# Kernel tuning notes

Measured on AMD Instinct MI355X. Metric: run time of the kernel, lower is better.

Reference implementation:

```python
import jax, jax.numpy as jnp
import numpy as np

D = 1024

def setup_inputs() -> dict:
    key = jax.random.key(0)
    ks = jax.random.split(key, 9)
    s = 1.0 / np.sqrt(D)
    x = jax.random.normal(ks[0], (4096, 8, D), dtype=jnp.float32)
    Wq = jax.random.uniform(ks[1], (D, D), jnp.float32, -s, s)
    bq = jax.random.uniform(ks[2], (D,), jnp.float32, -s, s)
    Wk = jax.random.uniform(ks[3], (D, D), jnp.float32, -s, s)
    bk = jax.random.uniform(ks[4], (D,), jnp.float32, -s, s)
    Wv = jax.random.uniform(ks[5], (D, D), jnp.float32, -s, s)
    bv = jax.random.uniform(ks[6], (D,), jnp.float32, -s, s)
    Wo = jax.random.uniform(ks[7], (D, D), jnp.float32, -s, s)
    bo = jax.random.uniform(ks[8], (D,), jnp.float32, -s, s)
    return {"x": x, "Wq": Wq, "bq": bq, "Wk": Wk, "bk": bk,
            "Wv": Wv, "bv": bv, "Wo": Wo, "bo": bo}

def reference(x, Wq, bq, Wk, bk, Wv, bv, Wo, bo):
    # x: (S, B, D) seq-first, matching torch module
    Q = jax.nn.elu(x @ Wq.T + bq) + 1.0  # (S,B,D)
    K = jax.nn.elu(x @ Wk.T + bk) + 1.0  # (S,B,D)
    V = x @ Wv.T + bv                    # (S,B,D)
    # KV = K^T V per batch: (B, D, D)
    KV = jnp.einsum('sbd,sbe->bde', K, V)
    # out = Q @ KV per batch, back to (S,B,D)
    out = jnp.einsum('sbd,bde->sbe', Q, KV)
    return out @ Wo.T + bo
```

## Files before the change

### kernel.cpp

```cpp
#include <hip/hip_runtime.h>


typedef __bf16 bf16;
typedef __attribute__((ext_vector_type(8))) __bf16 bf16x8;
typedef __attribute__((ext_vector_type(4))) __bf16 bf16x4;
typedef __attribute__((ext_vector_type(4))) float f32x4;

static constexpr int S = 4096;
static constexpr int B = 8;
static constexpr int D = 1024;
static constexpr int SB = S * B;
static constexpr long long NELEM = (long long)SB * D;

__device__ __forceinline__ void load_lds16(const bf16* g, void* l)
{
    __builtin_amdgcn_global_load_lds(
        (const __attribute__((address_space(1))) void*)g,
        (__attribute__((address_space(3))) void*)l, 16, 0, 0);
}

__global__ void cvt_f32_to_bf16(const float* __restrict__ in, bf16* __restrict__ out, int n)
{
    int i = (blockIdx.x * blockDim.x + threadIdx.x) * 4;
    int stride = gridDim.x * blockDim.x * 4;
    for (; i < n; i += stride) {
        float4 v = *(const float4*)(in + i);
        bf16x4 o;
        o[0] = (bf16)v.x; o[1] = (bf16)v.y; o[2] = (bf16)v.z; o[3] = (bf16)v.w;
        *(bf16x4*)(out + i) = o;
    }
}

__global__ __launch_bounds__(256) void cvt_transpose_1024(
    const float* __restrict__ in, bf16* __restrict__ out)
{
    __shared__ bf16 tile[64][72];
    const int e0 = blockIdx.y * 64;
    const int d0 = blockIdx.x * 64;
    const int t  = threadIdx.x;
    const int rl = t >> 3;
    const int c8 = (t & 7) * 8;
    #pragma unroll
    for (int p = 0; p < 2; ++p) {
        int r = rl + p * 32;
        float4 v0 = *(const float4*)(in + (long long)(e0 + r) * D + d0 + c8);
        float4 v1 = *(const float4*)(in + (long long)(e0 + r) * D + d0 + c8 + 4);
        tile[c8+0][r] = (bf16)v0.x; tile[c8+1][r] = (bf16)v0.y;
        tile[c8+2][r] = (bf16)v0.z; tile[c8+3][r] = (bf16)v0.w;
        tile[c8+4][r] = (bf16)v1.x; tile[c8+5][r] = (bf16)v1.y;
        tile[c8+6][r] = (bf16)v1.z; tile[c8+7][r] = (bf16)v1.w;
    }
    __syncthreads();
    #pragma unroll
    for (int p = 0; p < 2; ++p) {
        int dr = rl + p * 32;
        *(bf16x8*)(out + (long long)(d0 + dr) * D + e0 + c8) = *(bf16x8*)(&tile[dr][c8]);
    }
}

__global__ __launch_bounds__(256) void bvo_kernel(
    const float* __restrict__ Wo, const float* __restrict__ bv, float* __restrict__ bvo)
{
    const int row = blockIdx.x;
    const int t = threadIdx.x;
    float4 w = *(const float4*)(Wo + (long long)row * D + t * 4);
    float4 b = *(const float4*)(bv + t * 4);
    float s = w.x*b.x + w.y*b.y + w.z*b.z + w.w*b.w;
    __shared__ float red[256];
    red[t] = s; __syncthreads();
    for (int off = 128; off > 0; off >>= 1) {
        if (t < off) red[t] += red[t + off];
        __syncthreads();
    }
    if (t == 0) bvo[row] = red[0];
}

template<int BM, int BN, int WM, int WN, int EPI, int OUTF32, int BIASROW>
__global__ __launch_bounds__(WM * WN * 64, 2) void gemm_bt(
    const bf16* __restrict__ A, const bf16* __restrict__ Bm,
    const float* __restrict__ bias, void* __restrict__ Cout,
    int lda, int ldb, int ldc, int K,
    long long aBatch, long long bBatch, long long cBatch)
{
    constexpr int THREADS = WM * WN * 64;
    constexpr int WROWS = BM / WM, WCOLS = BN / WN;
    constexpr int MI = WROWS / 16, NI = WCOLS / 16;
    constexpr int ABYTES = BM * 64;
    constexpr int BBYTES = BN * 64;
    constexpr int BUF = ABYTES + BBYTES;

    __shared__ unsigned char smem[4 * BUF];

    const int tid  = threadIdx.x;
    const int lane = tid & 63;
    const int wave = tid >> 6;
    const int wr   = wave / WN;
    const int wc   = wave % WN;
    const int bz   = blockIdx.z;

    const int nx  = gridDim.x;
    const int bid = blockIdx.y * nx + blockIdx.x;
    const int cpx = (nx * gridDim.y) >> 3;
    const int swz = (bid & 7) * cpx + (bid >> 3);
    const long long m0 = (long long)(swz / nx) * BM;
    const long long n0 = (long long)(swz % nx) * BN;

    const bf16* Ab = A  + bz * aBatch + m0 * lda;
    const bf16* Bb = Bm + bz * bBatch + n0 * ldb;

    f32x4 acc[MI][NI] = {};
    const int NT = K >> 5;

    auto stage = [&](int t) {
        unsigned char* dst = smem + (t & 3) * BUF;
        const long long kk = (long long)t << 5;
        #pragma unroll
        for (int j = 0; j < 2; ++j) {
            const int g  = wave * 64 + lane + j * THREADS;
            const int gs = g ^ ((g >> 3) & 3);
            const int row = gs >> 2, col = (gs & 3) * 8;
            load_lds16(Ab + (long long)row * lda + kk + col,
                       dst + (wave * 64 + j * THREADS) * 16);
        }
        #pragma unroll
        for (int j = 0; j < 2; ++j) {
            const int g  = wave * 64 + lane + j * THREADS;
            const int gs = g ^ ((g >> 3) & 3);
            const int row = gs >> 2, col = (gs & 3) * 8;
            load_lds16(Bb + (long long)row * ldb + kk + col,
                       dst + ABYTES + (wave * 64 + j * THREADS) * 16);
        }
    };

    stage(0); stage(1); stage(2);

    const int ko2 = (lane >> 4) * 16;
    const int la15 = lane & 15;

    for (int t = 0; t < NT; ++t) {
        if (t + 2 < NT)      asm volatile("s_waitcnt vmcnt(8)" ::: "memory");
        else if (t + 1 < NT) asm volatile("s_waitcnt vmcnt(4)" ::: "memory");
        else                 asm volatile("s_waitcnt vmcnt(0)" ::: "memory");
        __builtin_amdgcn_s_barrier();
        asm volatile("" ::: "memory");

        if (t + 3 < NT) stage(t + 3);

        const unsigned char* buf = smem + (t & 3) * BUF;
        bf16x8 a[MI], b[NI];
        #pragma unroll
        for (int mi = 0; mi < MI; ++mi) {
            int ad = (wr * WROWS + mi * 16 + la15) * 64 + ko2;
            ad ^= ((ad >> 7) & 3) << 4;
            a[mi] = *(const bf16x8*)(buf + ad);
        }
        #pragma unroll
        for (int ni = 0; ni < NI; ++ni) {
            int ad = (wc * WCOLS + ni * 16 + la15) * 64 + ko2;
            ad ^= ((ad >> 7) & 3) << 4;
            b[ni] = *(const bf16x8*)(buf + ABYTES + ad);
        }

        __builtin_amdgcn_s_setprio(1);
        #pragma unroll
        for (int mi = 0; mi < MI; ++mi)
            #pragma unroll
            for (int ni = 0; ni < NI; ++ni)
                acc[mi][ni] = __builtin_amdgcn_mfma_f32_16x16x32_bf16(
                    a[mi], b[ni], acc[mi][ni], 0, 0, 0);
        __builtin_amdgcn_s_setprio(0);
    }

    const int crow = (lane >> 4) * 4;
    const int ccol = lane & 15;
    #pragma unroll
    for (int ni = 0; ni < NI; ++ni) {
        const long long c = n0 + wc * WCOLS + ni * 16 + ccol;
        float bcol = 0.0f;
        if (!BIASROW && bias) bcol = bias[c];
        #pragma unroll
        for (int mi = 0; mi < MI; ++mi) {
            const long long r0 = m0 + wr * WROWS + mi * 16 + crow;
            #pragma unroll
            for (int j = 0; j < 4; ++j) {
                float v = acc[mi][ni][j];
                v += BIASROW ? bias[r0 + j] : bcol;
                if (EPI == 1) v = (v > 0.0f) ? (v + 1.0f) : __expf(v);
                const long long idx = bz * cBatch + (r0 + j) * ldc + c;
                if (OUTF32) ((float*)Cout)[idx] = v;
                else        ((bf16*)Cout)[idx]  = (bf16)v;
            }
        }
    }
}

template<int EPI, int OUTF32, int BIASROW>
__global__ __launch_bounds__(512, 1) void gemm8p(
    const bf16* __restrict__ A, const bf16* __restrict__ Bm,
    const float* __restrict__ bias, void* __restrict__ Cout,
    int lda, int ldb, int ldc, int K,
    long long aBatch, long long bBatch, long long cBatch)
{
    __shared__ unsigned char smem[131072];

    const int tid  = threadIdx.x;
    const int lane = tid & 63;
    const int wave = tid >> 6;
    const int wr   = wave >> 2;
    const int wc   = wave & 3;
    const int bz   = blockIdx.z;

    const int nx  = gridDim.x;
    const int bid = blockIdx.y * nx + blockIdx.x;
    const int cpx = (nx * gridDim.y) >> 3;
    const int swzb = (bid & 7) * cpx + (bid >> 3);
    const long long m0 = (long long)(swzb / nx) * 256;
    const long long n0 = (long long)(swzb % nx) * 256;

    const bf16* Ab = A  + bz * aBatch + m0 * lda;
    const bf16* Bb = Bm + bz * bBatch + n0 * ldb;

    const int sg = (lane & 3) ^ ((lane >> 3) & 3);
    const long long srow = wave * 32 + (lane >> 2);
    const bf16* srcA = Ab + srow * lda + sg * 8;
    const bf16* srcB = Bb + srow * ldb + sg * 8;
    const int dstoff = wave * 2048;

    const int la15 = lane & 15;
    const int rsw  = (lane >> 4) ^ ((la15 >> 1) & 3);
    const int a16  = (wr * 128 + la15) * 4 + rsw;
    const int b16  = (wc * 64  + la15) * 4 + rsw;

    f32x4 acc[8][4] = {};
    const int NT = K >> 6;
    const int NI = NT >> 1;

    auto stageA = [&](int T, int kh) {
        const int reg = ((((T & 1) << 1) | kh) << 14);
        const long long kp = ((long long)T << 6) + (kh << 5);
        load_lds16(srcA + kp,            smem + reg + dstoff);
        load_lds16(srcA + kp + 16 * lda, smem + reg + dstoff + 1024);
    };
    auto stageB = [&](int T, int kh) {
        const int reg = 65536 + ((((T & 1) << 1) | kh) << 14);
        const long long kp = ((long long)T << 6) + (kh << 5);
        load_lds16(srcB + kp,            smem + reg + dstoff);
        load_lds16(srcB + kp + 16 * ldb, smem + reg + dstoff + 1024);
    };

    stageB(0, 0); stageA(0, 0); stageB(0, 1); stageA(0, 1);
    stageB(1, 0); stageA(1, 0); stageB(1, 1);
    asm volatile("s_waitcnt vmcnt(10)" ::: "memory");
    __builtin_amdgcn_s_barrier();
    __builtin_amdgcn_sched_barrier(0);

    bf16x8 bfr[4];
    for (int i = 0; i < NI; ++i) {
        const int t = 2 * i;
        const bool nl = (i + 1 < NI);
        #pragma unroll
        for (int p = 0; p < 8; ++p) {
            const int ks  = (p >> 1) & 1;
            const int ch  = p & 1;
            const int buf = p >> 2;
            const int regA = ((buf << 1) | ks) << 14;
            const int regB = 65536 + regA;

            bf16x8 afr[4];
            if (ch == 0) {
                #pragma unroll
                for (int ni = 0; ni < 4; ++ni)
                    bfr[ni] = *(const bf16x8*)(smem + regB + (b16 + ni * 64) * 16);
            }
            #pragma unroll
            for (int m4 = 0; m4 < 4; ++m4)
                afr[m4] = *(const bf16x8*)(smem + regA + (a16 + (ch * 4 + m4) * 64) * 16);

            if      (p == 0) stageA(t + 1, 1);
            else if (p == 1) { if (t + 2 < NT) stageB(t + 2, 0); }
            else if (p == 2) { if (t + 2 < NT) stageA(t + 2, 0); }
            else if (p == 3) { if (t + 2 < NT) stageB(t + 2, 1); }
            else if (p == 4) { if (t + 2 < NT) stageA(t + 2, 1); }
            else if (p == 5) { if (t + 3 < NT) stageB(t + 3, 0); }
            else if (p == 6) { if (t + 3 < NT) stageA(t + 3, 0); }
            else             { if (t + 3 < NT) stageB(t + 3, 1); }

            if (p == 1) {
                if (nl) asm volatile("s_waitcnt vmcnt(10)" ::: "memory");
                else    asm volatile("s_waitcnt vmcnt(8)"  ::: "memory");
            } else if (p == 3) {
                if (nl) asm volatile("s_waitcnt vmcnt(10)" ::: "memory");
                else    asm volatile("s_waitcnt vmcnt(4)"  ::: "memory");
            } else if (p == 5) {
                if (nl) asm volatile("s_waitcnt vmcnt(10)" ::: "memory");
                else    asm volatile("s_waitcnt vmcnt(0)"  ::: "memory");
            } else if (p == 7) {
                if (nl) asm volatile("s_waitcnt vmcnt(10)" ::: "memory");
            }

            __builtin_amdgcn_s_barrier();
            asm volatile("s_waitcnt lgkmcnt(0)" ::: "memory");
            __builtin_amdgcn_s_setprio(1);
            #pragma unroll
            for (int m4 = 0; m4 < 4; ++m4)
                #pragma unroll
                for (int ni = 0; ni < 4; ++ni)
                    acc[ch * 4 + m4][ni] = __builtin_amdgcn_mfma_f32_16x16x32_bf16(
                        afr[m4], bfr[ni], acc[ch * 4 + m4][ni], 0, 0, 0);
            __builtin_amdgcn_s_setprio(0);
            __builtin_amdgcn_s_barrier();
            __builtin_amdgcn_sched_barrier(0);
        }
    }

    const int crow = (lane >> 4) * 4;
    #pragma unroll
    for (int ni = 0; ni < 4; ++ni) {
        const long long c = n0 + wc * 64 + ni * 16 + la15;
        float bcol = 0.0f;
        if (!BIASROW && bias) bcol = bias[c];
        #pragma unroll
        for (int mi = 0; mi < 8; ++mi) {
            const long long r0 = m0 + wr * 128 + mi * 16 + crow;
            #pragma unroll
            for (int j = 0; j < 4; ++j) {
                float v = acc[mi][ni][j];
                v += BIASROW ? bias[r0 + j] : bcol;
                if (EPI == 1) v = (v > 0.0f) ? (v + 1.0f) : __expf(v);
                const long long idx = bz * cBatch + (r0 + j) * ldc + c;
                if (OUTF32) ((float*)Cout)[idx] = v;
                else        ((bf16*)Cout)[idx]  = (bf16)v;
            }
        }
    }
}

extern "C" void kernel_launch(void* const* d_in, const int* in_sizes, int n_in,
                              void* d_out, int out_size, void* d_ws, size_t ws_size,
                              hipStream_t stream)
{
    const float* x  = (const float*)d_in[0];
    const float* Wq = (const float*)d_in[1];
    const float* bq = (const float*)d_in[2];
    const float* Wk = (const float*)d_in[3];
    const float* bk = (const float*)d_in[4];
    const float* Wv = (const float*)d_in[5];
    const float* bv = (const float*)d_in[6];
    const float* Wo = (const float*)d_in[7];
    const float* bo = (const float*)d_in[8];
    float* out = (float*)d_out;

    char* ws = (char*)d_ws;
    if (ws_size < (size_t)159383552) return;
    bf16*  xb   = (bf16*)(ws + 0);
    bf16*  Qb   = (bf16*)(ws + 67108864);
    bf16*  Wvo  = (bf16*)(ws + 67108864);
    float* bvo  = (float*)(ws + 67108864 + 2097152);
    bf16*  KVo  = (bf16*)(ws + 134217728);
    bf16*  wqb  = (bf16*)(ws + 150994944);
    bf16*  wkb  = wqb + 1048576;
    bf16*  wob  = wkb + 1048576;
    bf16*  wvT  = wob + 1048576;
    bf16*  Kt   = (bf16*)d_out;
    bf16*  Vt   = Kt + NELEM;

    cvt_f32_to_bf16<<<4096, 256, 0, stream>>>(x,  xb,  (int)NELEM);
    cvt_f32_to_bf16<<<1024, 256, 0, stream>>>(Wq, wqb, D * D);
    cvt_f32_to_bf16<<<1024, 256, 0, stream>>>(Wk, wkb, D * D);
    cvt_f32_to_bf16<<<1024, 256, 0, stream>>>(Wo, wob, D * D);
    cvt_transpose_1024<<<dim3(16, 16), 256, 0, stream>>>(Wv, wvT);
    bvo_kernel<<<1024, 256, 0, stream>>>(Wo, bv, bvo);

    gemm_bt<128, 128, 2, 2, 0, 0, 0><<<dim3(8, 8, 1), 256, 0, stream>>>(
        wob, wvT, nullptr, Wvo, D, D, D, D, 0, 0, 0);

    gemm8p<1, 0, 1><<<dim3(16, 4, 8), 512, 0, stream>>>(
        wkb, xb, bk, Kt, D, B * D, S, D, 0, (long long)D, (long long)D * S);

    gemm8p<0, 0, 1><<<dim3(16, 4, 8), 512, 0, stream>>>(
        Wvo, xb, bvo, Vt, D, B * D, S, D, 0, (long long)D, (long long)D * S);

    gemm8p<1, 0, 0><<<dim3(4, 128, 1), 512, 0, stream>>>(
        xb, wqb, bq, Qb, D, D, D, D, 0, 0, 0);

    gemm_bt<128, 128, 2, 2, 0, 0, 0><<<dim3(8, 8, 8), 256, 0, stream>>>(
        Vt, Kt, nullptr, KVo, S, S, D, S,
        (long long)D * S, (long long)D * S, (long long)D * D);

    gemm8p<0, 1, 0><<<dim3(4, 16, 8), 512, 0, stream>>>(
        Qb, KVo, bo, out, B * D, D, B * D, D,
        (long long)D, (long long)D * D, (long long)D);
}
```

Baseline: 509.8 us.

## Fuse K and V projections into one GEMM and split-K the KV product

```diff
diff --git a/kernel.cpp b/kernel.cpp
--- a/kernel.cpp
+++ b/kernel.cpp
@@ -75,6 +75,19 @@
     if (t == 0) bvo[row] = red[0];
 }
 
+__global__ __launch_bounds__(256) void kv_add(const bf16* __restrict__ p, bf16* __restrict__ o)
+{
+    const long long DD = (long long)D * D;
+    const int b = blockIdx.y;
+    const long long i = ((long long)blockIdx.x * 256 + threadIdx.x) * 8;
+    bf16x8 u = *(const bf16x8*)(p + (2 * b) * DD + i);
+    bf16x8 v = *(const bf16x8*)(p + (2 * b + 1) * DD + i);
+    bf16x8 r;
+    #pragma unroll
+    for (int j = 0; j < 8; ++j) r[j] = (bf16)((float)u[j] + (float)v[j]);
+    *(bf16x8*)(o + b * DD + i) = r;
+}
+
 template<int BM, int BN, int WM, int WN, int EPI, int OUTF32, int BIASROW>
 __global__ __launch_bounds__(WM * WN * 64, 2) void gemm_bt(
     const bf16* __restrict__ A, const bf16* __restrict__ Bm,
@@ -194,7 +207,7 @@
     }
 }
 
-template<int EPI, int OUTF32, int BIASROW>
+template<int EPI, int OUTF32, int BIASROW, int SPLITK>
 __global__ __launch_bounds__(512, 1) void gemm8p(
     const bf16* __restrict__ A, const bf16* __restrict__ Bm,
     const float* __restrict__ bias, void* __restrict__ Cout,
@@ -208,7 +221,9 @@
     const int wave = tid >> 6;
     const int wr   = wave >> 2;
     const int wc   = wave & 3;
-    const int bz   = blockIdx.z;
+    const int bz    = blockIdx.z;
+    const int batch = bz / SPLITK;
+    const int kseg  = bz % SPLITK;
 
     const int nx  = gridDim.x;
     const int bid = blockIdx.y * nx + blockIdx.x;
@@ -217,8 +232,8 @@
     const long long m0 = (long long)(swzb / nx) * 256;
     const long long n0 = (long long)(swzb % nx) * 256;
 
-    const bf16* Ab = A  + bz * aBatch + m0 * lda;
-    const bf16* Bb = Bm + bz * bBatch + n0 * ldb;
+    const bf16* Ab = A  + batch * aBatch + m0 * lda + (long long)kseg * K;
+    const bf16* Bb = Bm + batch * bBatch + n0 * ldb + (long long)kseg * K;
 
     const int sg = (lane & 3) ^ ((lane >> 3) & 3);
     const long long srow = wave * 32 + (lane >> 2);
@@ -286,16 +301,11 @@
             else             { if (t + 3 < NT) stageB(t + 3, 1); }
 
             if (p == 1) {
-                if (nl) asm volatile("s_waitcnt vmcnt(10)" ::: "memory");
-                else    asm volatile("s_waitcnt vmcnt(8)"  ::: "memory");
-            } else if (p == 3) {
-                if (nl) asm volatile("s_waitcnt vmcnt(10)" ::: "memory");
-                else    asm volatile("s_waitcnt vmcnt(4)"  ::: "memory");
+                if (nl) asm volatile("s_waitcnt vmcnt(6)" ::: "memory");
+                else    asm volatile("s_waitcnt vmcnt(4)" ::: "memory");
             } else if (p == 5) {
-                if (nl) asm volatile("s_waitcnt vmcnt(10)" ::: "memory");
-                else    asm volatile("s_waitcnt vmcnt(0)"  ::: "memory");
-            } else if (p == 7) {
-                if (nl) asm volatile("s_waitcnt vmcnt(10)" ::: "memory");
+                if (nl) asm volatile("s_waitcnt vmcnt(6)" ::: "memory");
+                else    asm volatile("s_waitcnt vmcnt(0)" ::: "memory");
             }
 
             __builtin_amdgcn_s_barrier();
@@ -313,6 +323,8 @@
         }
     }
 
+    const bool doElu = (EPI == 1) || (EPI == 2 && m0 < 1024);
+    const long long cb = (long long)bz * cBatch;
     const int crow = (lane >> 4) * 4;
     #pragma unroll
     for (int ni = 0; ni < 4; ++ni) {
@@ -322,14 +334,22 @@
         #pragma unroll
         for (int mi = 0; mi < 8; ++mi) {
             const long long r0 = m0 + wr * 128 + mi * 16 + crow;
-            #pragma unroll
-            for (int j = 0; j < 4; ++j) {
-                float v = acc[mi][ni][j];
-                v += BIASROW ? bias[r0 + j] : bcol;
-                if (EPI == 1) v = (v > 0.0f) ? (v + 1.0f) : __expf(v);
-                const long long idx = bz * cBatch + (r0 + j) * ldc + c;
-                if (OUTF32) ((float*)Cout)[idx] = v;
-                else        ((bf16*)Cout)[idx]  = (bf16)v;
+            if (OUTF32) {
+                float* p = (float*)Cout + cb + r0 * ldc + c;
+                #pragma unroll
+                for (int j = 0; j < 4; ++j) {
+                    float v = acc[mi][ni][j] + (BIASROW ? bias[r0 + j] : bcol);
+                    if (doElu) v = (v > 0.0f) ? (v + 1.0f) : __expf(v);
+                    *p = v; p += ldc;
+                }
+            } else {
+                bf16* p = (bf16*)Cout + cb + r0 * ldc + c;
+                #pragma unroll
+                for (int j = 0; j < 4; ++j) {
+                    float v = acc[mi][ni][j] + (BIASROW ? bias[r0 + j] : bcol);
+                    if (doElu) v = (v > 0.0f) ? (v + 1.0f) : __expf(v);
+                    *p = (bf16)v; p += ldc;
+                }
             }
         }
     }
@@ -353,41 +373,41 @@
     char* ws = (char*)d_ws;
     if (ws_size < (size_t)159383552) return;
     bf16*  xb   = (bf16*)(ws + 0);
+    bf16*  part = (bf16*)(ws + 67108864);
     bf16*  Qb   = (bf16*)(ws + 67108864);
-    bf16*  Wvo  = (bf16*)(ws + 67108864);
-    float* bvo  = (float*)(ws + 67108864 + 2097152);
+    bf16*  wvT  = (bf16*)(ws + 134217728);
+    float* bkvo = (float*)(ws + 134217728 + 2097152);
     bf16*  KVo  = (bf16*)(ws + 134217728);
     bf16*  wqb  = (bf16*)(ws + 150994944);
-    bf16*  wkb  = wqb + 1048576;
-    bf16*  wob  = wkb + 1048576;
-    bf16*  wvT  = wob + 1048576;
-    bf16*  Kt   = (bf16*)d_out;
-    bf16*  Vt   = Kt + NELEM;
+    bf16*  wob  = wqb + 1048576;
+    bf16*  wkvo = wob + 1048576;
+    bf16*  KVb  = (bf16*)d_out;
 
     cvt_f32_to_bf16<<<4096, 256, 0, stream>>>(x,  xb,  (int)NELEM);
     cvt_f32_to_bf16<<<1024, 256, 0, stream>>>(Wq, wqb, D * D);
-    cvt_f32_to_bf16<<<1024, 256, 0, stream>>>(Wk, wkb, D * D);
     cvt_f32_to_bf16<<<1024, 256, 0, stream>>>(Wo, wob, D * D);
+    cvt_f32_to_bf16<<<1024, 256, 0, stream>>>(Wk, wkvo, D * D);
     cvt_transpose_1024<<<dim3(16, 16), 256, 0, stream>>>(Wv, wvT);
-    bvo_kernel<<<1024, 256, 0, stream>>>(Wo, bv, bvo);
+    bvo_kernel<<<1024, 256, 0, stream>>>(Wo, bv, bkvo + 1024);
+    hipMemcpyAsync(bkvo, bk, D * sizeof(float), hipMemcpyDeviceToDevice, stream);
 
     gemm_bt<128, 128, 2, 2, 0, 0, 0><<<dim3(8, 8, 1), 256, 0, stream>>>(
-        wob, wvT, nullptr, Wvo, D, D, D, D, 0, 0, 0);
-
-    gemm8p<1, 0, 1><<<dim3(16, 4, 8), 512, 0, stream>>>(
-        wkb, xb, bk, Kt, D, B * D, S, D, 0, (long long)D, (long long)D * S);
-
-    gemm8p<0, 0, 1><<<dim3(16, 4, 8), 512, 0, stream>>>(
-        Wvo, xb, bvo, Vt, D, B * D, S, D, 0, (long long)D, (long long)D * S);
-
-    gemm8p<1, 0, 0><<<dim3(4, 128, 1), 512, 0, stream>>>(
+        wob, wvT, nullptr, wkvo + (long long)1024 * 1024, D, D, D, D, 0, 0, 0);
+
+    gemm8p<2, 0, 1, 1><<<dim3(16, 8, 8), 512, 0, stream>>>(
+        wkvo, xb, bkvo, KVb, D, B * D, S, D,
+        0, (long long)D, (long long)2048 * S);
+
+    gemm8p<0, 0, 0, 2><<<dim3(4, 4, 16), 512, 0, stream>>>(
+        KVb + (long long)1024 * S, KVb, nullptr, part, S, S, D, 2048,
+        (long long)2048 * S, (long long)2048 * S, (long long)D * D);
+
+    kv_add<<<dim3(512, 8), 256, 0, stream>>>(part, KVo);
+
+    gemm8p<1, 0, 0, 1><<<dim3(4, 128, 1), 512, 0, stream>>>(
         xb, wqb, bq, Qb, D, D, D, D, 0, 0, 0);
 
-    gemm_bt<128, 128, 2, 2, 0, 0, 0><<<dim3(8, 8, 8), 256, 0, stream>>>(
-        Vt, Kt, nullptr, KVo, S, S, D, S,
-        (long long)D * S, (long long)D * S, (long long)D * D);
-
-    gemm8p<0, 1, 0><<<dim3(4, 16, 8), 512, 0, stream>>>(
+    gemm8p<0, 1, 0, 1><<<dim3(4, 16, 8), 512, 0, stream>>>(
         Qb, KVo, bo, out, B * D, D, B * D, D,
         (long long)D, (long long)D * D, (long long)D);
 }
```

Measured after the change: 538.0 us. 1.06x slower.
